# Kernel tuning notes

Measured on AMD Instinct MI355X. Metric: run time of the kernel, lower is better.

## Reference

```python
import jax, jax.numpy as jnp
import numpy as np

N = 50000
E = 600000


def setup_inputs() -> dict:
    key = jax.random.key(0)
    ks = jax.random.split(key, 8)
    x = jax.random.normal(ks[0], (N, 128), dtype=jnp.float32)
    # guarantee every node appears at least once as a source (row) so deg > 0
    row_extra = jax.random.randint(ks[1], (E - N,), 0, N, dtype=jnp.int32)
    row = jnp.concatenate([jnp.arange(N, dtype=jnp.int32), row_extra])
    col = jax.random.randint(ks[2], (E,), 0, N, dtype=jnp.int32)
    edge_index = jnp.stack([row, col])  # [2, E]
    edge_weight = jax.random.uniform(ks[3], (E,), dtype=jnp.float32, minval=0.1, maxval=1.0)
    s1 = 1.0 / np.sqrt(128)
    W1 = jax.random.normal(ks[4], (128, 128), dtype=jnp.float32) * s1
    b1 = jnp.zeros((128,), dtype=jnp.float32)
    W2 = jax.random.normal(ks[5], (128, 128), dtype=jnp.float32) * s1
    b2 = jnp.zeros((128,), dtype=jnp.float32)
    return {"x": x, "edge_index": edge_index, "edge_weight": edge_weight,
            "W1": W1, "b1": b1, "W2": W2, "b2": b2}


def _gcn_layer(x, row, col, edge_weight, W, b):
    # dense linear (torch Linear: x @ W.T + b)
    h = x @ W.T + b  # [N, d_out]
    n = h.shape[0]
    # degree via scatter-add of edge weights over source nodes
    deg = jax.ops.segment_sum(edge_weight, row, num_segments=n)  # [N]
    deg_inv_sqrt = deg ** -0.5
    norm = deg_inv_sqrt[row] * edge_weight * deg_inv_sqrt[col]  # [E]
    # message: gather source features, scale, scatter-add to targets
    msg = norm[:, None] * h[row]  # [E, d_out]
    return jax.ops.segment_sum(msg, col, num_segments=n)  # [N, d_out]


def reference(x, edge_index, edge_weight, W1, b1, W2, b2):
    row, col = edge_index[0], edge_index[1]
    h = _gcn_layer(x, row, col, edge_weight, W1, b1)
    h = jax.nn.relu(h)
    return _gcn_layer(h, row, col, edge_weight, W2, b2)
```

## Files before the change

kernel.cpp:

```cpp
#include <hip/hip_runtime.h>

#define DF 128
#define CAP 40

#define FMA4(a4, s, v)                                              \
    a4.x = fmaf(s, v.x, a4.x); a4.y = fmaf(s, v.y, a4.y);           \
    a4.z = fmaf(s, v.z, a4.z); a4.w = fmaf(s, v.w, a4.w)

__device__ __forceinline__ float4 agg_tail(const float4* __restrict__ H4,
                                           const int2* __restrict__ bucket,
                                           int i, int m,
                                           const float* __restrict__ deg,
                                           int t, float4 acc)
{
    for (; i + 4 <= m; i += 4) {
        const int4* b4 = (const int4*)(bucket + i);
        const int4 p0 = b4[0];
        const int4 p1 = b4[1];
        const float4 h0 = H4[(size_t)p0.x * 32 + t];
        const float4 h1 = H4[(size_t)p0.z * 32 + t];
        const float4 h2 = H4[(size_t)p1.x * 32 + t];
        const float4 h3 = H4[(size_t)p1.z * 32 + t];
        const float s0 = __int_as_float(p0.y) * rsqrtf(deg[p0.x]);
        const float s1 = __int_as_float(p0.w) * rsqrtf(deg[p0.z]);
        const float s2 = __int_as_float(p1.y) * rsqrtf(deg[p1.x]);
        const float s3 = __int_as_float(p1.w) * rsqrtf(deg[p1.z]);
        FMA4(acc, s0, h0);
        FMA4(acc, s1, h1);
        FMA4(acc, s2, h2);
        FMA4(acc, s3, h3);
    }
    for (; i < m; ++i) {
        const int2 rec = bucket[i];
        const float sv = __int_as_float(rec.y) * rsqrtf(deg[rec.x]);
        const float4 hv = H4[(size_t)rec.x * 32 + t];
        FMA4(acc, sv, hv);
    }
    return acc;
}

__device__ __forceinline__ void agg2(const float4* __restrict__ H4,
                                     const int2* __restrict__ bA, int mA,
                                     const int2* __restrict__ bB, int mB,
                                     const float* __restrict__ deg, int t,
                                     float4& accA, float4& accB)
{
    const int mc = mA < mB ? mA : mB;
    int i = 0;
    for (; i + 4 <= mc; i += 4) {
        const int4 a0 = ((const int4*)(bA + i))[0];
        const int4 a1 = ((const int4*)(bA + i))[1];
        const int4 c0 = ((const int4*)(bB + i))[0];
        const int4 c1 = ((const int4*)(bB + i))[1];
        const float4 hA0 = H4[(size_t)a0.x * 32 + t];
        const float4 hA1 = H4[(size_t)a0.z * 32 + t];
        const float4 hA2 = H4[(size_t)a1.x * 32 + t];
        const float4 hA3 = H4[(size_t)a1.z * 32 + t];
        const float4 hB0 = H4[(size_t)c0.x * 32 + t];
        const float4 hB1 = H4[(size_t)c0.z * 32 + t];
        const float4 hB2 = H4[(size_t)c1.x * 32 + t];
        const float4 hB3 = H4[(size_t)c1.z * 32 + t];
        const float sA0 = __int_as_float(a0.y) * rsqrtf(deg[a0.x]);
        const float sA1 = __int_as_float(a0.w) * rsqrtf(deg[a0.z]);
        const float sA2 = __int_as_float(a1.y) * rsqrtf(deg[a1.x]);
        const float sA3 = __int_as_float(a1.w) * rsqrtf(deg[a1.z]);
        const float sB0 = __int_as_float(c0.y) * rsqrtf(deg[c0.x]);
        const float sB1 = __int_as_float(c0.w) * rsqrtf(deg[c0.z]);
        const float sB2 = __int_as_float(c1.y) * rsqrtf(deg[c1.x]);
        const float sB3 = __int_as_float(c1.w) * rsqrtf(deg[c1.z]);
        FMA4(accA, sA0, hA0);
        FMA4(accA, sA1, hA1);
        FMA4(accA, sA2, hA2);
        FMA4(accA, sA3, hA3);
        FMA4(accB, sB0, hB0);
        FMA4(accB, sB1, hB1);
        FMA4(accB, sB2, hB2);
        FMA4(accB, sB3, hB3);
    }
    accA = agg_tail(H4, bA, i, mA, deg, t, accA);
    accB = agg_tail(H4, bB, i, mB, deg, t, accB);
}

template <int RPT>
__device__ __forceinline__ void gemm_from_lds(
    float* __restrict__ Xs, float* __restrict__ Wsk,
    const float* __restrict__ W, const float* __restrict__ b,
    float* __restrict__ H, int nrows, int n0, int tid)
{
    const int rgrp = tid >> 5;
    const int cgrp = tid & 31;

    float4 acc[RPT];
    const float4 bias = ((const float4*)b)[cgrp];
#pragma unroll
    for (int r = 0; r < RPT; ++r) acc[r] = bias;

    const float4* Xs4 = (const float4*)Xs;
    const float4* Ws4 = (const float4*)Wsk;

    for (int k0 = 0; k0 < DF; k0 += 32) {
        __syncthreads();
#pragma unroll
        for (int i = 0; i < 4; ++i) {
            int idx = tid + i * 256;
            int c   = idx >> 3;
            int kk  = idx & 7;
            float4 v = ((const float4*)(W + (size_t)c * DF + k0))[kk];
            int kb = kk * 4;
            Wsk[(kb + 0) * DF + c] = v.x;
            Wsk[(kb + 1) * DF + c] = v.y;
            Wsk[(kb + 2) * DF + c] = v.z;
            Wsk[(kb + 3) * DF + c] = v.w;
        }
        __syncthreads();

#pragma unroll
        for (int kk = 0; kk < 8; ++kk) {
            const int kb = (k0 >> 2) + kk;
            float4 w0 = Ws4[(kk * 4 + 0) * 32 + cgrp];
            float4 w1 = Ws4[(kk * 4 + 1) * 32 + cgrp];
            float4 w2 = Ws4[(kk * 4 + 2) * 32 + cgrp];
            float4 w3 = Ws4[(kk * 4 + 3) * 32 + cgrp];
#pragma unroll
            for (int r = 0; r < RPT; ++r) {
                float4 x4 = Xs4[(rgrp * RPT + r) * 32 + kb];
                acc[r].x = fmaf(x4.x, w0.x, acc[r].x);
                acc[r].y = fmaf(x4.x, w0.y, acc[r].y);
                acc[r].z = fmaf(x4.x, w0.z, acc[r].z);
                acc[r].w = fmaf(x4.x, w0.w, acc[r].w);
                acc[r].x = fmaf(x4.y, w1.x, acc[r].x);
                acc[r].y = fmaf(x4.y, w1.y, acc[r].y);
                acc[r].z = fmaf(x4.y, w1.z, acc[r].z);
                acc[r].w = fmaf(x4.y, w1.w, acc[r].w);
                acc[r].x = fmaf(x4.z, w2.x, acc[r].x);
                acc[r].y = fmaf(x4.z, w2.y, acc[r].y);
                acc[r].z = fmaf(x4.z, w2.z, acc[r].z);
                acc[r].w = fmaf(x4.z, w2.w, acc[r].w);
                acc[r].x = fmaf(x4.w, w3.x, acc[r].x);
                acc[r].y = fmaf(x4.w, w3.y, acc[r].y);
                acc[r].z = fmaf(x4.w, w3.z, acc[r].z);
                acc[r].w = fmaf(x4.w, w3.w, acc[r].w);
            }
        }
    }

#pragma unroll
    for (int r = 0; r < RPT; ++r) {
        int n = n0 + rgrp * RPT + r;
        if (n < nrows) ((float4*)(H + (size_t)n * DF))[cgrp] = acc[r];
    }
}

__global__ __launch_bounds__(256) void build_gemm_kernel(
    const float* __restrict__ X, const float* __restrict__ W,
    const float* __restrict__ b, float* __restrict__ H, int nrows,
    const int* __restrict__ row, const int* __restrict__ col,
    const float* __restrict__ ew,
    float* __restrict__ deg, int* __restrict__ cnt, int2* __restrict__ csr,
    int E, int gemmBlocks)
{
    __shared__ float Xs[64 * DF];
    __shared__ float Wsk[32 * DF];

    const int tid = threadIdx.x;

    if (blockIdx.x >= gemmBlocks) {
        int e = (blockIdx.x - gemmBlocks) * 256 + tid;
        if (e < E) {
            int r = row[e], c = col[e];
            float wv = ew[e];
            atomicAdd(&deg[r], wv);
            int pos = atomicAdd(&cnt[c], 1);
            if (pos < CAP)
                csr[(size_t)c * CAP + pos] = make_int2(r, __float_as_int(wv));
        }
        return;
    }

    const int n0 = blockIdx.x * 64;
#pragma unroll
    for (int i = 0; i < 8; ++i) {
        int idx = tid + i * 256;
        int r   = idx >> 5;
        int kk  = idx & 31;
        int n   = n0 + r;
        float4 v = make_float4(0.f, 0.f, 0.f, 0.f);
        if (n < nrows) v = ((const float4*)(X + (size_t)n * DF))[kk];
        ((float4*)Xs)[idx] = v;
    }
    gemm_from_lds<8>(Xs, Wsk, W, b, H, nrows, n0, tid);
}

__global__ __launch_bounds__(256, 4) void agg_gemm_kernel(
    const float4* __restrict__ H4,
    const int2* __restrict__ csr, const int* __restrict__ cnt,
    const float* __restrict__ deg,
    const float* __restrict__ W, const float* __restrict__ b,
    float* __restrict__ O, int N)
{
    __shared__ float Xs[32 * DF];
    __shared__ float Wsk[32 * DF];

    const int tid = threadIdx.x;
    const int g   = tid >> 5;
    const int t   = tid & 31;
    const int n0  = blockIdx.x * 32;

#pragma unroll
    for (int jp = 0; jp < 2; ++jp) {
        const int rA = g * 4 + jp * 2;
        const int rB = rA + 1;
        const int nodeA = n0 + rA;
        const int nodeB = n0 + rB;
        int mA = 0, mB = 0;
        if (nodeA < N) { mA = cnt[nodeA]; if (mA > CAP) mA = CAP; }
        if (nodeB < N) { mB = cnt[nodeB]; if (mB > CAP) mB = CAP; }
        float4 accA = make_float4(0.f, 0.f, 0.f, 0.f);
        float4 accB = make_float4(0.f, 0.f, 0.f, 0.f);
        agg2(H4, csr + (size_t)nodeA * CAP, mA,
                 csr + (size_t)nodeB * CAP, mB, deg, t, accA, accB);
        if (nodeA < N) {
            const float d = rsqrtf(deg[nodeA]);
            accA.x = fmaxf(accA.x * d, 0.f); accA.y = fmaxf(accA.y * d, 0.f);
            accA.z = fmaxf(accA.z * d, 0.f); accA.w = fmaxf(accA.w * d, 0.f);
        }
        if (nodeB < N) {
            const float d = rsqrtf(deg[nodeB]);
            accB.x = fmaxf(accB.x * d, 0.f); accB.y = fmaxf(accB.y * d, 0.f);
            accB.z = fmaxf(accB.z * d, 0.f); accB.w = fmaxf(accB.w * d, 0.f);
        }
        ((float4*)Xs)[rA * 32 + t] = accA;
        ((float4*)Xs)[rB * 32 + t] = accB;
    }
    gemm_from_lds<4>(Xs, Wsk, W, b, O, N, n0, tid);
}

__global__ __launch_bounds__(256) void agg_kernel(
    const float4* __restrict__ H4,
    const int2* __restrict__ csr, const int* __restrict__ cnt,
    const float* __restrict__ deg,
    float4* __restrict__ O4, int N)
{
    const int gid  = blockIdx.x * blockDim.x + threadIdx.x;
    const int half = gid >> 5;
    const int t    = gid & 31;
    const int nA   = half * 2;
    const int nB   = nA + 1;
    if (nA >= N) return;
    int mA = cnt[nA]; if (mA > CAP) mA = CAP;
    int mB = 0;
    if (nB < N) { mB = cnt[nB]; if (mB > CAP) mB = CAP; }
    float4 accA = make_float4(0.f, 0.f, 0.f, 0.f);
    float4 accB = make_float4(0.f, 0.f, 0.f, 0.f);
    agg2(H4, csr + (size_t)nA * CAP, mA,
             csr + (size_t)nB * CAP, mB, deg, t, accA, accB);
    const float dA = rsqrtf(deg[nA]);
    accA.x *= dA; accA.y *= dA; accA.z *= dA; accA.w *= dA;
    O4[(size_t)nA * 32 + t] = accA;
    if (nB < N) {
        const float dB = rsqrtf(deg[nB]);
        accB.x *= dB; accB.y *= dB; accB.z *= dB; accB.w *= dB;
        O4[(size_t)nB * 32 + t] = accB;
    }
}

extern "C" void kernel_launch(void* const* d_in, const int* in_sizes, int n_in,
                              void* d_out, int out_size, void* d_ws, size_t ws_size,
                              hipStream_t stream) {
    const float* x  = (const float*)d_in[0];
    const int*   ei = (const int*)d_in[1];
    const float* ew = (const float*)d_in[2];
    const float* W1 = (const float*)d_in[3];
    const float* b1 = (const float*)d_in[4];
    const float* W2 = (const float*)d_in[5];
    const float* b2 = (const float*)d_in[6];
    float* out = (float*)d_out;

    const int E = in_sizes[2];
    const int N = in_sizes[0] / DF;
    const int* row = ei;
    const int* col = ei + E;

    char* ws = (char*)d_ws;
    size_t offb = 0;
    auto alloc = [&](size_t bytes) { char* p = ws + offb; offb = (offb + bytes + 511) & ~(size_t)511; return p; };
    float* deg  = (float*)alloc((size_t)2 * N * 4);
    int*   cnt  = (int*)(deg + N);
    int2*  csr  = (int2*)alloc((size_t)N * CAP * 8);
    float* h1   = (float*)alloc((size_t)N * DF * 4);
    float* h2   = (float*)alloc((size_t)N * DF * 4);
    (void)ws_size;

    hipMemsetAsync(deg, 0, (size_t)2 * N * 4, stream);

    const int TB = 256;
    const int eblocks = (E + TB - 1) / TB;
    const int gemm1_blocks = (N + 63) / 64;
    const int agg_gemm_blocks = (N + 31) / 32;

    build_gemm_kernel<<<gemm1_blocks + eblocks, 256, 0, stream>>>(
        x, W1, b1, h1, N, row, col, ew, deg, cnt, csr, E, gemm1_blocks);

    agg_gemm_kernel<<<agg_gemm_blocks, 256, 0, stream>>>(
        (const float4*)h1, csr, cnt, deg, W2, b2, h2, N);

    const int pairs = (N + 1) / 2;
    const int agg_blocks = (pairs * 32 + TB - 1) / TB;
    agg_kernel<<<agg_blocks, TB, 0, stream>>>((const float4*)h2, csr, cnt, deg,
                                              (float4*)out, N);
}
```

Baseline: 281.6 us.

## Prescale layer-2 features by inverse sqrt degree and vectorize edge build

Measured after the change: 284.5 us. About the same (+1.0%).

```diff
diff --git a/kernel.cpp b/kernel.cpp
--- a/kernel.cpp
+++ b/kernel.cpp
@@ -7,6 +7,7 @@
     a4.x = fmaf(s, v.x, a4.x); a4.y = fmaf(s, v.y, a4.y);           \
     a4.z = fmaf(s, v.z, a4.z); a4.w = fmaf(s, v.w, a4.w)
 
+template <bool SCALED>
 __device__ __forceinline__ float4 agg_tail(const float4* __restrict__ H4,
                                            const int2* __restrict__ bucket,
                                            int i, int m,
@@ -21,10 +22,10 @@
         const float4 h1 = H4[(size_t)p0.z * 32 + t];
         const float4 h2 = H4[(size_t)p1.x * 32 + t];
         const float4 h3 = H4[(size_t)p1.z * 32 + t];
-        const float s0 = __int_as_float(p0.y) * rsqrtf(deg[p0.x]);
-        const float s1 = __int_as_float(p0.w) * rsqrtf(deg[p0.z]);
-        const float s2 = __int_as_float(p1.y) * rsqrtf(deg[p1.x]);
-        const float s3 = __int_as_float(p1.w) * rsqrtf(deg[p1.z]);
+        const float s0 = SCALED ? __int_as_float(p0.y) : __int_as_float(p0.y) * rsqrtf(deg[p0.x]);
+        const float s1 = SCALED ? __int_as_float(p0.w) : __int_as_float(p0.w) * rsqrtf(deg[p0.z]);
+        const float s2 = SCALED ? __int_as_float(p1.y) : __int_as_float(p1.y) * rsqrtf(deg[p1.x]);
+        const float s3 = SCALED ? __int_as_float(p1.w) : __int_as_float(p1.w) * rsqrtf(deg[p1.z]);
         FMA4(acc, s0, h0);
         FMA4(acc, s1, h1);
         FMA4(acc, s2, h2);
@@ -32,13 +33,14 @@
     }
     for (; i < m; ++i) {
         const int2 rec = bucket[i];
-        const float sv = __int_as_float(rec.y) * rsqrtf(deg[rec.x]);
+        const float sv = SCALED ? __int_as_float(rec.y) : __int_as_float(rec.y) * rsqrtf(deg[rec.x]);
         const float4 hv = H4[(size_t)rec.x * 32 + t];
         FMA4(acc, sv, hv);
     }
     return acc;
 }
 
+template <bool SCALED>
 __device__ __forceinline__ void agg2(const float4* __restrict__ H4,
                                      const int2* __restrict__ bA, int mA,
                                      const int2* __restrict__ bB, int mB,
@@ -60,14 +62,14 @@
         const float4 hB1 = H4[(size_t)c0.z * 32 + t];
         const float4 hB2 = H4[(size_t)c1.x * 32 + t];
         const float4 hB3 = H4[(size_t)c1.z * 32 + t];
-        const float sA0 = __int_as_float(a0.y) * rsqrtf(deg[a0.x]);
-        const float sA1 = __int_as_float(a0.w) * rsqrtf(deg[a0.z]);
-        const float sA2 = __int_as_float(a1.y) * rsqrtf(deg[a1.x]);
-        const float sA3 = __int_as_float(a1.w) * rsqrtf(deg[a1.z]);
-        const float sB0 = __int_as_float(c0.y) * rsqrtf(deg[c0.x]);
-        const float sB1 = __int_as_float(c0.w) * rsqrtf(deg[c0.z]);
-        const float sB2 = __int_as_float(c1.y) * rsqrtf(deg[c1.x]);
-        const float sB3 = __int_as_float(c1.w) * rsqrtf(deg[c1.z]);
+        const float sA0 = SCALED ? __int_as_float(a0.y) : __int_as_float(a0.y) * rsqrtf(deg[a0.x]);
+        const float sA1 = SCALED ? __int_as_float(a0.w) : __int_as_float(a0.w) * rsqrtf(deg[a0.z]);
+        const float sA2 = SCALED ? __int_as_float(a1.y) : __int_as_float(a1.y) * rsqrtf(deg[a1.x]);
+        const float sA3 = SCALED ? __int_as_float(a1.w) : __int_as_float(a1.w) * rsqrtf(deg[a1.z]);
+        const float sB0 = SCALED ? __int_as_float(c0.y) : __int_as_float(c0.y) * rsqrtf(deg[c0.x]);
+        const float sB1 = SCALED ? __int_as_float(c0.w) : __int_as_float(c0.w) * rsqrtf(deg[c0.z]);
+        const float sB2 = SCALED ? __int_as_float(c1.y) : __int_as_float(c1.y) * rsqrtf(deg[c1.x]);
+        const float sB3 = SCALED ? __int_as_float(c1.w) : __int_as_float(c1.w) * rsqrtf(deg[c1.z]);
         FMA4(accA, sA0, hA0);
         FMA4(accA, sA1, hA1);
         FMA4(accA, sA2, hA2);
@@ -77,15 +79,16 @@
         FMA4(accB, sB2, hB2);
         FMA4(accB, sB3, hB3);
     }
-    accA = agg_tail(H4, bA, i, mA, deg, t, accA);
-    accB = agg_tail(H4, bB, i, mB, deg, t, accB);
-}
-
-template <int RPT>
+    accA = agg_tail<SCALED>(H4, bA, i, mA, deg, t, accA);
+    accB = agg_tail<SCALED>(H4, bB, i, mB, deg, t, accB);
+}
+
+template <int RPT, bool SCALE_OUT>
 __device__ __forceinline__ void gemm_from_lds(
     float* __restrict__ Xs, float* __restrict__ Wsk,
     const float* __restrict__ W, const float* __restrict__ b,
-    float* __restrict__ H, int nrows, int n0, int tid)
+    float* __restrict__ H, int nrows, int n0, int tid,
+    const float* __restrict__ degv)
 {
     const int rgrp = tid >> 5;
     const int cgrp = tid & 31;
@@ -147,11 +150,17 @@
 #pragma unroll
     for (int r = 0; r < RPT; ++r) {
         int n = n0 + rgrp * RPT + r;
-        if (n < nrows) ((float4*)(H + (size_t)n * DF))[cgrp] = acc[r];
-    }
-}
-
-__global__ __launch_bounds__(256) void build_gemm_kernel(
+        if (n < nrows) {
+            if (SCALE_OUT) {
+                const float d = rsqrtf(degv[n]);
+                acc[r].x *= d; acc[r].y *= d; acc[r].z *= d; acc[r].w *= d;
+            }
+            ((float4*)(H + (size_t)n * DF))[cgrp] = acc[r];
+        }
+    }
+}
+
+__global__ __launch_bounds__(256, 4) void build_gemm_kernel(
     const float* __restrict__ X, const float* __restrict__ W,
     const float* __restrict__ b, float* __restrict__ H, int nrows,
     const int* __restrict__ row, const int* __restrict__ col,
@@ -159,27 +168,46 @@
     float* __restrict__ deg, int* __restrict__ cnt, int2* __restrict__ csr,
     int E, int gemmBlocks)
 {
-    __shared__ float Xs[64 * DF];
+    __shared__ float Xs[32 * DF];
     __shared__ float Wsk[32 * DF];
 
     const int tid = threadIdx.x;
 
     if (blockIdx.x >= gemmBlocks) {
-        int e = (blockIdx.x - gemmBlocks) * 256 + tid;
-        if (e < E) {
-            int r = row[e], c = col[e];
-            float wv = ew[e];
-            atomicAdd(&deg[r], wv);
-            int pos = atomicAdd(&cnt[c], 1);
-            if (pos < CAP)
-                csr[(size_t)c * CAP + pos] = make_int2(r, __float_as_int(wv));
+        const int g  = (blockIdx.x - gemmBlocks) * 256 + tid;
+        const int e0 = g * 4;
+        if (e0 + 3 < E) {
+            const int4   r4 = ((const int4*)row)[g];
+            const int4   c4 = ((const int4*)col)[g];
+            const float4 w4 = ((const float4*)ew)[g];
+            const int p0 = atomicAdd(&cnt[c4.x], 1);
+            const int p1 = atomicAdd(&cnt[c4.y], 1);
+            const int p2 = atomicAdd(&cnt[c4.z], 1);
+            const int p3 = atomicAdd(&cnt[c4.w], 1);
+            atomicAdd(&deg[r4.x], w4.x);
+            atomicAdd(&deg[r4.y], w4.y);
+            atomicAdd(&deg[r4.z], w4.z);
+            atomicAdd(&deg[r4.w], w4.w);
+            if (p0 < CAP) csr[(size_t)c4.x * CAP + p0] = make_int2(r4.x, __float_as_int(w4.x));
+            if (p1 < CAP) csr[(size_t)c4.y * CAP + p1] = make_int2(r4.y, __float_as_int(w4.y));
+            if (p2 < CAP) csr[(size_t)c4.z * CAP + p2] = make_int2(r4.z, __float_as_int(w4.z));
+            if (p3 < CAP) csr[(size_t)c4.w * CAP + p3] = make_int2(r4.w, __float_as_int(w4.w));
+        } else {
+            for (int e = e0; e < E; ++e) {
+                const int r = row[e], c = col[e];
+                const float wv = ew[e];
+                atomicAdd(&deg[r], wv);
+                const int pos = atomicAdd(&cnt[c], 1);
+                if (pos < CAP)
+                    csr[(size_t)c * CAP + pos] = make_int2(r, __float_as_int(wv));
+            }
         }
         return;
     }
 
-    const int n0 = blockIdx.x * 64;
-#pragma unroll
-    for (int i = 0; i < 8; ++i) {
+    const int n0 = blockIdx.x * 32;
+#pragma unroll
+    for (int i = 0; i < 4; ++i) {
         int idx = tid + i * 256;
         int r   = idx >> 5;
         int kk  = idx & 31;
@@ -188,7 +216,7 @@
         if (n < nrows) v = ((const float4*)(X + (size_t)n * DF))[kk];
         ((float4*)Xs)[idx] = v;
     }
-    gemm_from_lds<8>(Xs, Wsk, W, b, H, nrows, n0, tid);
+    gemm_from_lds<4, false>(Xs, Wsk, W, b, H, nrows, n0, tid, nullptr);
 }
 
 __global__ __launch_bounds__(256, 4) void agg_gemm_kernel(
@@ -217,8 +245,8 @@
         if (nodeB < N) { mB = cnt[nodeB]; if (mB > CAP) mB = CAP; }
         float4 accA = make_float4(0.f, 0.f, 0.f, 0.f);
         float4 accB = make_float4(0.f, 0.f, 0.f, 0.f);
-        agg2(H4, csr + (size_t)nodeA * CAP, mA,
-                 csr + (size_t)nodeB * CAP, mB, deg, t, accA, accB);
+        agg2<false>(H4, csr + (size_t)nodeA * CAP, mA,
+                        csr + (size_t)nodeB * CAP, mB, deg, t, accA, accB);
         if (nodeA < N) {
             const float d = rsqrtf(deg[nodeA]);
             accA.x = fmaxf(accA.x * d, 0.f); accA.y = fmaxf(accA.y * d, 0.f);
@@ -232,7 +260,7 @@
         ((float4*)Xs)[rA * 32 + t] = accA;
         ((float4*)Xs)[rB * 32 + t] = accB;
     }
-    gemm_from_lds<4>(Xs, Wsk, W, b, O, N, n0, tid);
+    gemm_from_lds<4, true>(Xs, Wsk, W, b, O, N, n0, tid, deg);
 }
 
 __global__ __launch_bounds__(256) void agg_kernel(
@@ -252,8 +280,8 @@
     if (nB < N) { mB = cnt[nB]; if (mB > CAP) mB = CAP; }
     float4 accA = make_float4(0.f, 0.f, 0.f, 0.f);
     float4 accB = make_float4(0.f, 0.f, 0.f, 0.f);
-    agg2(H4, csr + (size_t)nA * CAP, mA,
-             csr + (size_t)nB * CAP, mB, deg, t, accA, accB);
+    agg2<true>(H4, csr + (size_t)nA * CAP, mA,
+                   csr + (size_t)nB * CAP, mB, deg, t, accA, accB);
     const float dA = rsqrtf(deg[nA]);
     accA.x *= dA; accA.y *= dA; accA.z *= dA; accA.w *= dA;
     O4[(size_t)nA * 32 + t] = accA;
@@ -294,14 +322,14 @@
     hipMemsetAsync(deg, 0, (size_t)2 * N * 4, stream);
 
     const int TB = 256;
-    const int eblocks = (E + TB - 1) / TB;
-    const int gemm1_blocks = (N + 63) / 64;
-    const int agg_gemm_blocks = (N + 31) / 32;
-
-    build_gemm_kernel<<<gemm1_blocks + eblocks, 256, 0, stream>>>(
-        x, W1, b1, h1, N, row, col, ew, deg, cnt, csr, E, gemm1_blocks);
-
-    agg_gemm_kernel<<<agg_gemm_blocks, 256, 0, stream>>>(
+    const int ethreads = (E + 3) / 4;
+    const int eblocks = (ethreads + TB - 1) / TB;
+    const int gemm_blocks = (N + 31) / 32;
+
+    build_gemm_kernel<<<gemm_blocks + eblocks, 256, 0, stream>>>(
+        x, W1, b1, h1, N, row, col, ew, deg, cnt, csr, E, gemm_blocks);
+
+    agg_gemm_kernel<<<gemm_blocks, 256, 0, stream>>>(
         (const float4*)h1, csr, cnt, deg, W2, b2, h2, N);
 
     const int pairs = (N + 1) / 2;
```
